# Kernel optimization log

Hardware: AMD Instinct MI355X
Metric: run time of the kernel (lower is better)

Reference implementation:

```python
import jax, jax.numpy as jnp
import numpy as np

BETA = 0.9  # snntorch Leaky beta (single-step, zero init mem => mem = x)
H = 8       # num_heads
EPS = 1e-5

@jax.custom_vjp
def lif_spike(x):
    # snn.Leaky single step, mem init 0: mem = BETA*0 + x ; spk = heaviside(mem - 1.0)
    return (x > 1.0).astype(x.dtype)

def _lif_fwd(x):
    return lif_spike(x), x

def _lif_bwd(x, g):
    # ATan surrogate (snntorch default, alpha=2): d spk/d mem = 1/(1 + (pi*(mem-1))^2)
    u = x - 1.0
    return (g / (1.0 + (jnp.pi * u) ** 2),)

lif_spike.defvjp(_lif_fwd, _lif_bwd)

def layer_norm(x, g, b):
    m = jnp.mean(x, -1, keepdims=True)
    v = jnp.mean((x - m) ** 2, -1, keepdims=True)
    return (x - m) * jax.lax.rsqrt(v + EPS) * g + b

def mha(x, Wqkv, Wo, causal):
    B, N, D = x.shape
    hd = D // H
    q, k, v = jnp.split(x @ Wqkv, 3, axis=-1)
    q = q.reshape(B, N, H, hd).transpose(0, 2, 1, 3)
    k = k.reshape(B, N, H, hd).transpose(0, 2, 1, 3)
    v = v.reshape(B, N, H, hd).transpose(0, 2, 1, 3)
    s = jnp.einsum('bhqd,bhkd->bhqk', q, k) / jnp.sqrt(jnp.asarray(hd, x.dtype))
    if causal:
        s = jnp.where(jnp.tril(jnp.ones((N, N), bool)), s, jnp.asarray(-1e9, x.dtype))
    a = jax.nn.softmax(s, axis=-1)
    o = jnp.einsum('bhqk,bhkd->bhqd', a, v).transpose(0, 2, 1, 3).reshape(B, N, D)
    return o @ Wo

def transformer(x, qkv, out, ln1, ff1, ff2, ln2, causal):
    # pre-norm transformer blocks; Encoder non-causal, Decoder causal
    for i in range(qkv.shape[0]):
        x = x + mha(layer_norm(x, ln1[i, 0], ln1[i, 1]), qkv[i], out[i], causal)
        x = x + jax.nn.gelu(layer_norm(x, ln2[i, 0], ln2[i, 1]) @ ff1[i]) @ ff2[i]
    return x

def setup_inputs():
    key = jax.random.key(0)
    B, R, S, D = 8, 90, 240, 256
    enc_depth, pred_depth = 8, 6
    ks = iter(jax.random.split(key, 64))
    def nrm(shape, std):
        return jax.random.normal(next(ks), shape, jnp.float32) * std
    def enc_params(depth):
        return dict(
            qkv=nrm((depth, D, 3 * D), 0.05),
            out=nrm((depth, D, D), 0.05),
            ln1=jnp.stack([jnp.ones((depth, D)), jnp.zeros((depth, D))], 1),
            ff1=nrm((depth, D, 4 * D), 0.05),
            ff2=nrm((depth, 4 * D, D), 0.05),
            ln2=jnp.stack([jnp.ones((depth, D)), jnp.zeros((depth, D))], 1),
        )
    t, s_, p = enc_params(enc_depth), enc_params(enc_depth), enc_params(pred_depth)
    inp = dict(
        x=jax.random.normal(next(ks), (B, R, S), jnp.float32),
        W_embed=nrm((S, D), 0.1), b_embed=jnp.zeros((D,), jnp.float32),
        pos_embedding=nrm((1, R, D), 1.0),
        mask_token=nrm((1, 1, D), 0.02),
        norm_g=jnp.ones((D,), jnp.float32), norm_b=jnp.zeros((D,), jnp.float32),
        W_dec=nrm((D, S), 0.1), b_dec=jnp.zeros((S,), jnp.float32),
    )
    for name, prm in (('t', t), ('s', s_), ('p', p)):
        for k2, v2 in prm.items():
            inp[name + '_' + k2] = v2
    return inp

def reference(x, W_embed, b_embed, pos_embedding, mask_token, norm_g, norm_b, W_dec, b_dec,
              t_qkv, t_out, t_ln1, t_ff1, t_ff2, t_ln2,
              s_qkv, s_out, s_ln1, s_ff1, s_ff2, s_ln2,
              p_qkv, p_out, p_ln1, p_ff1, p_ff2, p_ln2):
    B, R, S = x.shape
    D = W_embed.shape[1]
    # token embed + pos + token_lif
    x_emb = lif_spike(x @ W_embed + b_embed + pos_embedding)  # [B,R,D]
    # teacher (torch.no_grad)
    teacher_full = lif_spike(layer_norm(
        transformer(x_emb, t_qkv, t_out, t_ln1, t_ff1, t_ff2, t_ln2, False), norm_g, norm_b))
    teacher_full = jax.lax.stop_gradient(teacher_full)
    # student
    student_full = lif_spike(layer_norm(
        transformer(x_emb, s_qkv, s_out, s_ln1, s_ff1, s_ff2, s_ln2, False), norm_g, norm_b))
    # batched exhaustive leave-one-out: for each target t, context = all rows != t
    loo = np.stack([np.delete(np.arange(R), t) for t in range(R)])  # [R, R-1]
    ctx = student_full[:, loo, :]                                   # [B,R,R-1,D]
    masks = lif_spike(mask_token + pos_embedding)                   # [1,R,D] mask_lif
    masks = jnp.broadcast_to(masks[:, :, None, :], (B, R, 1, D))
    seq = jnp.concatenate([ctx, masks], axis=2).reshape(B * R, R, D)
    pred = lif_spike(transformer(seq, p_qkv, p_out, p_ln1, p_ff1, p_ff2, p_ln2, True))
    pred_targets = pred[:, -1, :].reshape(B, R, D)  # last token = predicted target region
    teacher_targets = teacher_full                   # exhaustive: targets are all R rows in order
    pred_seq = lif_spike(pred_targets @ W_dec + b_dec)      # output_lif [B,R,S]
    teacher_seq = lif_spike(teacher_targets @ W_dec + b_dec)
    target_seq = x
    return (pred_seq, teacher_seq, target_seq,
            pred_seq.mean(-1), teacher_seq.mean(-1), target_seq.mean(-1))
```

## Files before the change

kernel.cpp:

```cpp
#include <hip/hip_runtime.h>
#include <math.h>


__device__ __forceinline__ float gelu_f(float x) {
    const float c = 0.7978845608028654f;
    float x3 = x * x * x;
    float inner = c * (x + 0.044715f * x3);
    return 0.5f * x * (1.0f + tanhf(inner));
}

__device__ __forceinline__ int suffix_off(int g) {
    int b = g / 90, r = g - b * 90;
    return b * 4095 + 90 * r - ((r * (r - 1)) >> 1);
}

__global__ __launch_bounds__(256) void embed_kernel(
    const float* __restrict__ x, const float* __restrict__ We,
    const float* __restrict__ be, const float* __restrict__ pos,
    float* __restrict__ xemb) {
    int tok = blockIdx.x;
    int d = threadIdx.x;
    __shared__ float xs[240];
    if (d < 240) xs[d] = x[(size_t)tok * 240 + d];
    __syncthreads();
    int r = tok % 90;
    double acc = 0.0;
    for (int s = 0; s < 240; ++s)
        acc = fma((double)xs[s], (double)We[(size_t)s * 256 + d], acc);
    float a = (float)acc + be[d] + pos[r * 256 + d];
    xemb[(size_t)tok * 256 + d] = (a > 1.0f) ? 1.0f : 0.0f;
}

__global__ void copy_kernel(float* __restrict__ dst, const float* __restrict__ src, int n) {
    int i = blockIdx.x * 256 + threadIdx.x;
    if (i < n) dst[i] = src[i];
}
__global__ void zero_kernel(float* __restrict__ p, int n) {
    int i = blockIdx.x * 256 + threadIdx.x;
    if (i < n) p[i] = 0.f;
}

__global__ __launch_bounds__(256) void ln_kernel(
    const float* __restrict__ X,
    const float* __restrict__ gA, const float* __restrict__ bA,
    const float* __restrict__ gB, const float* __restrict__ bB,
    int split, float* __restrict__ Y) {
    int row = blockIdx.x;
    int d = threadIdx.x;
    const float* g = (row < split) ? gA : gB;
    const float* b = (row < split) ? bA : bB;
    __shared__ float red[256];
    float v = X[(size_t)row * 256 + d];
    red[d] = v;
    __syncthreads();
    for (int s = 128; s > 0; s >>= 1) { if (d < s) red[d] += red[d + s]; __syncthreads(); }
    float mean = red[0] * (1.0f / 256.0f);
    __syncthreads();
    float dv = v - mean;
    red[d] = dv * dv;
    __syncthreads();
    for (int s = 128; s > 0; s >>= 1) { if (d < s) red[d] += red[d + s]; __syncthreads(); }
    float var = red[0] * (1.0f / 256.0f);
    float r = 1.0f / sqrtf(var + 1e-5f);
    Y[(size_t)row * 256 + d] = dv * r * g[d] + b[d];
}

__global__ __launch_bounds__(256) void ln_lif_kernel(
    const float* __restrict__ X, const float* __restrict__ g, const float* __restrict__ b,
    float* __restrict__ Y) {
    int row = blockIdx.x;
    int d = threadIdx.x;
    __shared__ float red[256];
    float v = X[(size_t)row * 256 + d];
    red[d] = v;
    __syncthreads();
    for (int s = 128; s > 0; s >>= 1) { if (d < s) red[d] += red[d + s]; __syncthreads(); }
    float mean = red[0] * (1.0f / 256.0f);
    __syncthreads();
    float dv = v - mean;
    red[d] = dv * dv;
    __syncthreads();
    for (int s = 128; s > 0; s >>= 1) { if (d < s) red[d] += red[d + s]; __syncthreads(); }
    float var = red[0] * (1.0f / 256.0f);
    float r = 1.0f / sqrtf(var + 1e-5f);
    float val = dv * r * g[d] + b[d];
    Y[(size_t)row * 256 + d] = (val > 1.0f) ? 1.0f : 0.0f;
}

#define BM 64
#define BN 64
#define BK 16
template <int EPI>
__global__ __launch_bounds__(256) void gemm_kernel(
    const float* __restrict__ A, const float* __restrict__ W0,
    const float* __restrict__ W1, int wsplit,
    float* __restrict__ C, const float* __restrict__ R,
    int M, int N, int K, int ldA, int ldW, int ldC,
    int zA, int zW, long zC) {
    __shared__ float As[BK][BM + 4];
    __shared__ float Ws[BK][BN];
    int bm = blockIdx.y * BM;
    int bn = blockIdx.x * BN;
    int z = blockIdx.z;
    A += (size_t)z * zA;
    const float* W = ((bm < wsplit) ? W0 : W1) + (size_t)z * zW;
    C += (size_t)z * zC;
    const float* Rp = R + (size_t)z * zC;
    int tid = threadIdx.x;
    int tx = tid & 15;
    int ty = tid >> 4;
    float acc[4][4] = {{0.f}};
    for (int k0 = 0; k0 < K; k0 += BK) {
        {
            int r = tid >> 2;
            int kk = (tid & 3) * 4;
            int gm = bm + r;
            float4 v = make_float4(0.f, 0.f, 0.f, 0.f);
            if (gm < M) v = *(const float4*)(A + (size_t)gm * ldA + k0 + kk);
            As[kk + 0][r] = v.x; As[kk + 1][r] = v.y;
            As[kk + 2][r] = v.z; As[kk + 3][r] = v.w;
        }
        {
            int kk = tid >> 4;
            int n = (tid & 15) * 4;
            float4 v = *(const float4*)(W + (size_t)(k0 + kk) * ldW + bn + n);
            *(float4*)&Ws[kk][n] = v;
        }
        __syncthreads();
        #pragma unroll
        for (int k = 0; k < BK; ++k) {
            float a[4], w[4];
            #pragma unroll
            for (int i = 0; i < 4; ++i) a[i] = As[k][ty * 4 + i];
            #pragma unroll
            for (int j = 0; j < 4; ++j) w[j] = Ws[k][tx * 4 + j];
            #pragma unroll
            for (int i = 0; i < 4; ++i)
                #pragma unroll
                for (int j = 0; j < 4; ++j)
                    acc[i][j] = fmaf(a[i], w[j], acc[i][j]);
        }
        __syncthreads();
    }
    #pragma unroll
    for (int i = 0; i < 4; ++i) {
        int gm = bm + ty * 4 + i;
        if (gm >= M) continue;
        #pragma unroll
        for (int j = 0; j < 4; ++j) {
            int gn = bn + tx * 4 + j;
            float v = acc[i][j];
            if (EPI == 1) v += Rp[(size_t)gm * ldC + gn];
            if (EPI == 2) v = gelu_f(v);
            C[(size_t)gm * ldC + gn] = v;
        }
    }
}

__global__ void addff_kernel(float4* __restrict__ X, const float4* __restrict__ S,
                             long zstr4, int n4) {
    int i = blockIdx.x * 256 + threadIdx.x;
    if (i >= n4) return;
    float4 x = X[i];
    float4 s0 = S[i], s1 = S[i + zstr4], s2 = S[i + 2 * zstr4], s3 = S[i + 3 * zstr4];
    x.x = (((x.x + s0.x) + s1.x) + s2.x) + s3.x;
    x.y = (((x.y + s0.y) + s1.y) + s2.y) + s3.y;
    x.z = (((x.z + s0.z) + s1.z) + s2.z) + s3.z;
    x.w = (((x.w + s0.w) + s1.w) + s2.w) + s3.w;
    X[i] = x;
}

__global__ __launch_bounds__(128) void attn_kernel(
    const float* __restrict__ QKV, float* __restrict__ AO,
    int N, int causal, int hs, int off2) {
    int s = blockIdx.x, h = blockIdx.y;
    int tokbase = (s < hs) ? s * N : off2 + (s - hs) * N;
    __shared__ float Ks[90][32];
    __shared__ float Vs[90][32];
    int tid = threadIdx.x;
    for (int i = tid; i < N * 32; i += 128) {
        int n = i >> 5, d = i & 31;
        size_t base = ((size_t)(tokbase + n)) * 768 + h * 32;
        Ks[n][d] = QKV[base + 256 + d];
        Vs[n][d] = QKV[base + 512 + d];
    }
    __syncthreads();
    int q = tid;
    if (q >= N) return;
    float qv[32];
    size_t qbase = ((size_t)(tokbase + q)) * 768 + h * 32;
    #pragma unroll
    for (int d = 0; d < 32; ++d) qv[d] = QKV[qbase + d];
    const float sq = 5.656854249492380195f;
    int kmax = causal ? (q + 1) : N;
    float m = -3.0e38f;
    for (int k = 0; k < kmax; ++k) {
        float sd = 0.f;
        #pragma unroll
        for (int d = 0; d < 32; ++d) sd = fmaf(qv[d], Ks[k][d], sd);
        sd /= sq;
        m = fmaxf(m, sd);
    }
    float sum = 0.f;
    float acc[32];
    #pragma unroll
    for (int d = 0; d < 32; ++d) acc[d] = 0.f;
    for (int k = 0; k < kmax; ++k) {
        float sd = 0.f;
        #pragma unroll
        for (int d = 0; d < 32; ++d) sd = fmaf(qv[d], Ks[k][d], sd);
        sd /= sq;
        float p = expf(sd - m);
        sum += p;
        #pragma unroll
        for (int d = 0; d < 32; ++d) acc[d] = fmaf(p, Vs[k][d], acc[d]);
    }
    size_t obase = ((size_t)(tokbase + q)) * 256 + h * 32;
    #pragma unroll
    for (int d = 0; d < 32; ++d) AO[obase + d] = acc[d] / sum;
}

__global__ __launch_bounds__(128) void suffix_attn_kernel(
    const float* __restrict__ QKV, const float* __restrict__ kv,
    float* __restrict__ AO, int g0) {
    int ls = blockIdx.x, h = blockIdx.y;
    int g = g0 + ls;
    int b = g / 90, r = g - b * 90;
    int toff = suffix_off(g) - suffix_off(g0);
    int L = 90 - r;
    __shared__ float Ks[90][32];
    __shared__ float Vs[90][32];
    int tid = threadIdx.x;
    for (int i = tid; i < 90 * 32; i += 128) {
        int p = i >> 5, d = i & 31;
        float kk, vv;
        if (p < r) {
            const float* src = kv + ((size_t)(b * 89 + p)) * 512 + h * 32 + d;
            kk = src[0]; vv = src[256];
        } else {
            size_t base = ((size_t)(toff + p - r)) * 768 + h * 32 + d;
            kk = QKV[base + 256]; vv = QKV[base + 512];
        }
        Ks[p][d] = kk; Vs[p][d] = vv;
    }
    __syncthreads();
    if (tid >= L) return;
    int jq = r + tid;
    float qv[32];
    size_t qbase = ((size_t)(toff + tid)) * 768 + h * 32;
    #pragma unroll
    for (int d = 0; d < 32; ++d) qv[d] = QKV[qbase + d];
    const float sq = 5.656854249492380195f;
    int kmax = jq + 1;
    float m = -3.0e38f;
    for (int k = 0; k < kmax; ++k) {
        float sd = 0.f;
        #pragma unroll
        for (int d = 0; d < 32; ++d) sd = fmaf(qv[d], Ks[k][d], sd);
        sd /= sq;
        m = fmaxf(m, sd);
    }
    float sum = 0.f;
    float acc[32];
    #pragma unroll
    for (int d = 0; d < 32; ++d) acc[d] = 0.f;
    for (int k = 0; k < kmax; ++k) {
        float sd = 0.f;
        #pragma unroll
        for (int d = 0; d < 32; ++d) sd = fmaf(qv[d], Ks[k][d], sd);
        sd /= sq;
        float p = expf(sd - m);
        sum += p;
        #pragma unroll
        for (int d = 0; d < 32; ++d) acc[d] = fmaf(p, Vs[k][d], acc[d]);
    }
    size_t obase = ((size_t)(toff + tid)) * 256 + h * 32;
    #pragma unroll
    for (int d = 0; d < 32; ++d) AO[obase + d] = acc[d] / sum;
}

__global__ void masks_kernel(const float* __restrict__ mt, const float* __restrict__ pos,
                             float* __restrict__ M) {
    int i = blockIdx.x * 256 + threadIdx.x;
    if (i >= 90 * 256) return;
    int d = i & 255;
    float v = mt[d] + pos[i];
    M[i] = (v > 1.0f) ? 1.0f : 0.0f;
}

__global__ __launch_bounds__(256) void gather_canon_kernel(
    const float* __restrict__ student, float* __restrict__ Xc, int b0) {
    int tc = blockIdx.x;
    int d = threadIdx.x;
    int b = b0 + tc / 89, p = tc % 89;
    Xc[(size_t)tc * 256 + d] = student[((size_t)(b * 90 + p)) * 256 + d];
}

__global__ __launch_bounds__(256) void kvcopy_kernel(
    const float* __restrict__ QKVc, float* __restrict__ kvl, int b0) {
    int tc = blockIdx.x;
    int c = threadIdx.x;
    size_t gtc = (size_t)b0 * 89 + tc;
    kvl[gtc * 512 + c]       = QKVc[(size_t)tc * 768 + 256 + c];
    kvl[gtc * 512 + 256 + c] = QKVc[(size_t)tc * 768 + 512 + c];
}

__global__ __launch_bounds__(256) void gather_suffix_kernel(
    const float* __restrict__ student, const float* __restrict__ masks,
    float* __restrict__ X, int g0) {
    int ls = blockIdx.x, slot = blockIdx.y;
    int d = threadIdx.x;
    int g = g0 + ls;
    int b = g / 90, r = g - b * 90;
    if (slot >= 90 - r) return;
    int j = r + slot;
    int dst = suffix_off(g) - suffix_off(g0) + slot;
    float v;
    if (j == 89) v = masks[r * 256 + d];
    else         v = student[((size_t)(b * 90 + j + 1)) * 256 + d];
    X[(size_t)dst * 256 + d] = v;
}

__global__ __launch_bounds__(256) void extract_suffix_kernel(
    const float* __restrict__ X, float* __restrict__ predT, int g0) {
    int ls = blockIdx.x;
    int d = threadIdx.x;
    int g = g0 + ls;
    int r = g % 90;
    int tok = suffix_off(g) - suffix_off(g0) + (89 - r);
    float v = X[(size_t)tok * 256 + d];
    predT[(size_t)g * 256 + d] = (v > 1.0f) ? 1.0f : 0.0f;
}

__global__ __launch_bounds__(256) void decode_kernel(
    const float* __restrict__ T, const float* __restrict__ Wd, const float* __restrict__ bd,
    float* __restrict__ outseq, float* __restrict__ outmean) {
    int row = blockIdx.x;
    int n = threadIdx.x;
    __shared__ float ts[256];
    __shared__ float red[256];
    ts[n] = T[(size_t)row * 256 + n];
    __syncthreads();
    float sval = 0.f;
    if (n < 240) {
        double acc = 0.0;
        for (int k = 0; k < 256; ++k)
            acc = fma((double)ts[k], (double)Wd[(size_t)k * 240 + n], acc);
        float a = (float)acc;
        a += bd[n];
        sval = (a > 1.0f) ? 1.0f : 0.0f;
        outseq[(size_t)row * 240 + n] = sval;
    }
    red[n] = sval;
    __syncthreads();
    for (int s = 128; s > 0; s >>= 1) { if (n < s) red[n] += red[n + s]; __syncthreads(); }
    if (n == 0) outmean[row] = red[0] * (1.0f / 240.0f);
}

__global__ __launch_bounds__(256) void target_kernel(
    const float* __restrict__ x, float* __restrict__ outseq, float* __restrict__ outmean) {
    int row = blockIdx.x;
    int n = threadIdx.x;
    __shared__ float red[256];
    float v = 0.f;
    if (n < 240) {
        v = x[(size_t)row * 240 + n];
        outseq[(size_t)row * 240 + n] = v;
    }
    red[n] = v;
    __syncthreads();
    for (int s = 128; s > 0; s >>= 1) { if (n < s) red[n] += red[n + s]; __syncthreads(); }
    if (n == 0) outmean[row] = red[0] * (1.0f / 240.0f);
}

extern "C" void kernel_launch(void* const* d_in, const int* in_sizes, int n_in,
                              void* d_out, int out_size, void* d_ws, size_t ws_size,
                              hipStream_t stream) {
    const float* x   = (const float*)d_in[0];
    const float* We  = (const float*)d_in[1];
    const float* be  = (const float*)d_in[2];
    const float* pos = (const float*)d_in[3];
    const float* mt  = (const float*)d_in[4];
    const float* ng  = (const float*)d_in[5];
    const float* nb  = (const float*)d_in[6];
    const float* Wd  = (const float*)d_in[7];
    const float* bd  = (const float*)d_in[8];
    const float* prm[3][6];
    for (int g = 0; g < 3; ++g)
        for (int k = 0; k < 6; ++k)
            prm[g][k] = (const float*)d_in[9 + g * 6 + k];

    float* wp = (float*)d_ws;
    auto alloc = [&](size_t n) { float* q = wp; wp += n; return q; };
    float* x_emb   = alloc(720 * 256);
    float* teacher = alloc(720 * 256);
    float* student = alloc(720 * 256);
    float* predT   = alloc(720 * 256);
    float* masksb  = alloc(90 * 256);
    float* kvc     = alloc(6ull * 712 * 512);
    size_t fixed = (size_t)(wp - (float*)d_ws);

    size_t avail = ws_size / 4;
    long tcap_l = 90;
    if (avail > fixed) {
        long t = (long)((avail - fixed) / 3328);
        if (t > tcap_l) tcap_l = t;
    }
    if (tcap_l > 32760) tcap_l = 32760;
    int TCAP = (int)tcap_l;
    float* X   = alloc((size_t)TCAP * 256);
    float* Xn  = alloc((size_t)TCAP * 256);
    float* QKV = alloc((size_t)TCAP * 768);
    float* H   = alloc((size_t)TCAP * 1024);
    float* S   = alloc(4ull * TCAP * 256);
    long  zS   = (long)TCAP * 256;
    bool co_batch = (TCAP >= 1488);

    float* out = (float*)d_out;
    const int NOSPLIT = 1 << 30;

    embed_kernel<<<720, 256, 0, stream>>>(x, We, be, pos, x_emb);
    masks_kernel<<<90, 256, 0, stream>>>(mt, pos, masksb);

    auto run_layer = [&](int T, int gA, int gB, int l, int split, auto&& attn_launch) {
        const float* qkvA = prm[gA][0] + (size_t)l * 256 * 768;
        const float* qkvB = prm[gB][0] + (size_t)l * 256 * 768;
        const float* woA  = prm[gA][1] + (size_t)l * 256 * 256;
        const float* woB  = prm[gB][1] + (size_t)l * 256 * 256;
        const float* l1A  = prm[gA][2] + (size_t)l * 512;
        const float* l1B  = prm[gB][2] + (size_t)l * 512;
        const float* f1A  = prm[gA][3] + (size_t)l * 256 * 1024;
        const float* f1B  = prm[gB][3] + (size_t)l * 256 * 1024;
        const float* f2A  = prm[gA][4] + (size_t)l * 1024 * 256;
        const float* f2B  = prm[gB][4] + (size_t)l * 1024 * 256;
        const float* l2A  = prm[gA][5] + (size_t)l * 512;
        const float* l2B  = prm[gB][5] + (size_t)l * 512;
        int gy = (T + 63) / 64;
        ln_kernel<<<T, 256, 0, stream>>>(X, l1A, l1A + 256, l1B, l1B + 256, split, Xn);
        gemm_kernel<0><<<dim3(12, gy, 1), 256, 0, stream>>>(
            Xn, qkvA, qkvB, split, QKV, QKV, T, 768, 256, 256, 768, 768, 0, 0, 0);
        attn_launch();
        gemm_kernel<1><<<dim3(4, gy, 1), 256, 0, stream>>>(
            Xn, woA, woB, split, X, X, T, 256, 256, 256, 256, 256, 0, 0, 0);
        ln_kernel<<<T, 256, 0, stream>>>(X, l2A, l2A + 256, l2B, l2B + 256, split, Xn);
        gemm_kernel<2><<<dim3(16, gy, 1), 256, 0, stream>>>(
            Xn, f1A, f1B, split, H, H, T, 1024, 256, 256, 1024, 1024, 0, 0, 0);
        gemm_kernel<0><<<dim3(4, gy, 4), 256, 0, stream>>>(
            H, f2A, f2B, split, S, S, T, 256, 256, 1024, 256, 256, 256, 65536, zS);
        addff_kernel<<<(T * 64 + 255) / 256, 256, 0, stream>>>(
            (float4*)X, (const float4*)S, zS / 4, T * 64);
    };

    if (co_batch) {
        copy_kernel<<<720, 256, 0, stream>>>(X, x_emb, 720 * 256);
        copy_kernel<<<720, 256, 0, stream>>>(X + 768 * 256, x_emb, 720 * 256);
        zero_kernel<<<48, 256, 0, stream>>>(X + 720 * 256, 48 * 256);
        for (int l = 0; l < 8; ++l)
            run_layer(1488, 0, 1, l, 768,
                      [&] { attn_kernel<<<dim3(16, 8), 128, 0, stream>>>(
                                QKV, Xn, 90, 0, 8, 768); });
        ln_lif_kernel<<<720, 256, 0, stream>>>(X, ng, nb, teacher);
        ln_lif_kernel<<<720, 256, 0, stream>>>(X + 768 * 256, ng, nb, student);
    } else {
        int ce = TCAP / 90; if (ce > 8) ce = 8; if (ce < 1) ce = 1;
        for (int gi = 0; gi < 2; ++gi) {
            for (int s0 = 0; s0 < 8; s0 += ce) {
                int c = (8 - s0) < ce ? (8 - s0) : ce;
                int T = c * 90;
                copy_kernel<<<(T * 256 + 255) / 256, 256, 0, stream>>>(
                    X, x_emb + (size_t)s0 * 90 * 256, T * 256);
                for (int l = 0; l < 8; ++l)
                    run_layer(T, gi, gi, l, NOSPLIT,
                              [&] { attn_kernel<<<dim3(c, 8), 128, 0, stream>>>(
                                        QKV, Xn, 90, 0, c, 0); });
                ln_lif_kernel<<<T, 256, 0, stream>>>(
                    X, ng, nb, (gi == 0 ? teacher : student) + (size_t)s0 * 90 * 256);
            }
        }
    }

    {
        int cb = TCAP / 89; if (cb > 8) cb = 8; if (cb < 1) cb = 1;
        for (int b0 = 0; b0 < 8; b0 += cb) {
            int c = (8 - b0) < cb ? (8 - b0) : cb;
            int T = c * 89;
            gather_canon_kernel<<<T, 256, 0, stream>>>(student, X, b0);
            for (int l = 0; l < 6; ++l) {
                float* kvl = kvc + (size_t)l * 712 * 512;
                run_layer(T, 2, 2, l, NOSPLIT,
                          [&] {
                              kvcopy_kernel<<<T, 256, 0, stream>>>(QKV, kvl, b0);
                              attn_kernel<<<dim3(c, 8), 128, 0, stream>>>(
                                  QKV, Xn, 89, 1, c, 0);
                          });
            }
        }
    }

    auto Toff = [](int g) { int b = g / 90, r = g - b * 90;
                            return (long)b * 4095 + 90L * r - (long)r * (r - 1) / 2; };
    int cs = TCAP / 90; if (cs < 1) cs = 1; if (cs > 720) cs = 720;
    for (int g0 = 0; g0 < 720; ) {
        int g1 = g0 + cs; if (g1 > 720) g1 = 720;
        while ((int)(Toff(g1) - Toff(g0)) > TCAP && g1 > g0 + 1) --g1;
        int c = g1 - g0;
        int Tc = (int)(Toff(g1) - Toff(g0));
        { dim3 g(c, 90);
          gather_suffix_kernel<<<g, 256, 0, stream>>>(student, masksb, X, g0); }
        for (int l = 0; l < 6; ++l) {
            float* kvl = kvc + (size_t)l * 712 * 512;
            run_layer(Tc, 2, 2, l, NOSPLIT,
                      [&] { dim3 g(c, 8);
                            suffix_attn_kernel<<<g, 128, 0, stream>>>(QKV, kvl, Xn, g0); });
        }
        extract_suffix_kernel<<<c, 256, 0, stream>>>(X, predT, g0);
        g0 = g1;
    }

    decode_kernel<<<720, 256, 0, stream>>>(predT, Wd, bd, out + 0, out + 518400);
    decode_kernel<<<720, 256, 0, stream>>>(teacher, Wd, bd, out + 172800, out + 519120);
    target_kernel<<<720, 256, 0, stream>>>(x, out + 345600, out + 519840);
}
```

Measured before the change: 9.874 ms.

## Compute only last-token rows in final predictor layer; double-buffer GEMM smem

The last predictor layer only matters at the final (mask) token, so the suffix path now runs QKV for all tokens but attention, output projection, LN2 and FFN only for the last row of each sequence, using a new single-query attention kernel. The canonical-prefix pass in the last layer now only computes K/V without the full layer. The GEMM kernel also gets register-prefetch double-buffering of shared-memory tiles to overlap global loads with FMA work. This adds workspace buffers and more launches per chunk, and the last-query attention uses a single thread per head, which may be slow.

```diff
diff --git a/kernel.cpp b/kernel.cpp
--- a/kernel.cpp
+++ b/kernel.cpp
@@ -87,8 +87,6 @@
     Y[(size_t)row * 256 + d] = (val > 1.0f) ? 1.0f : 0.0f;
 }
 
-#define BM 64
-#define BN 64
 #define BK 16
 template <int EPI>
 __global__ __launch_bounds__(256) void gemm_kernel(
@@ -97,10 +95,10 @@
     float* __restrict__ C, const float* __restrict__ R,
     int M, int N, int K, int ldA, int ldW, int ldC,
     int zA, int zW, long zC) {
-    __shared__ float As[BK][BM + 4];
-    __shared__ float Ws[BK][BN];
-    int bm = blockIdx.y * BM;
-    int bn = blockIdx.x * BN;
+    __shared__ float As[2][BK][64 + 4];
+    __shared__ float Ws[2][BK][64];
+    int bm = blockIdx.y * 64;
+    int bn = blockIdx.x * 64;
     int z = blockIdx.z;
     A += (size_t)z * zA;
     const float* W = ((bm < wsplit) ? W0 : W1) + (size_t)z * zW;
@@ -109,50 +107,63 @@
     int tid = threadIdx.x;
     int tx = tid & 15;
     int ty = tid >> 4;
+    int ar = tid >> 2;
+    int ak = (tid & 3) * 4;
+    int wk = tid >> 4;
+    int wn = (tid & 15) * 4;
+    int gm = bm + ar;
+    bool aok = gm < M;
+    const float* Aptr = A + (size_t)gm * ldA + ak;
+    const float* Wptr = W + (size_t)wk * ldW + bn + wn;
+
     float acc[4][4] = {{0.f}};
-    for (int k0 = 0; k0 < K; k0 += BK) {
-        {
-            int r = tid >> 2;
-            int kk = (tid & 3) * 4;
-            int gm = bm + r;
-            float4 v = make_float4(0.f, 0.f, 0.f, 0.f);
-            if (gm < M) v = *(const float4*)(A + (size_t)gm * ldA + k0 + kk);
-            As[kk + 0][r] = v.x; As[kk + 1][r] = v.y;
-            As[kk + 2][r] = v.z; As[kk + 3][r] = v.w;
-        }
-        {
-            int kk = tid >> 4;
-            int n = (tid & 15) * 4;
-            float4 v = *(const float4*)(W + (size_t)(k0 + kk) * ldW + bn + n);
-            *(float4*)&Ws[kk][n] = v;
-        }
-        __syncthreads();
+    float4 va = aok ? *(const float4*)Aptr : make_float4(0.f, 0.f, 0.f, 0.f);
+    float4 vw = *(const float4*)Wptr;
+    As[0][ak + 0][ar] = va.x; As[0][ak + 1][ar] = va.y;
+    As[0][ak + 2][ar] = va.z; As[0][ak + 3][ar] = va.w;
+    *(float4*)&Ws[0][wk][wn] = vw;
+    __syncthreads();
+
+    int nt = K / BK;
+    for (int t = 0; t < nt; ++t) {
+        int cur = t & 1;
+        if (t + 1 < nt) {
+            va = aok ? *(const float4*)(Aptr + (t + 1) * BK)
+                     : make_float4(0.f, 0.f, 0.f, 0.f);
+            vw = *(const float4*)(Wptr + (size_t)(t + 1) * BK * ldW);
+        }
         #pragma unroll
         for (int k = 0; k < BK; ++k) {
             float a[4], w[4];
             #pragma unroll
-            for (int i = 0; i < 4; ++i) a[i] = As[k][ty * 4 + i];
+            for (int i = 0; i < 4; ++i) a[i] = As[cur][k][ty * 4 + i];
             #pragma unroll
-            for (int j = 0; j < 4; ++j) w[j] = Ws[k][tx * 4 + j];
+            for (int j = 0; j < 4; ++j) w[j] = Ws[cur][k][tx * 4 + j];
             #pragma unroll
             for (int i = 0; i < 4; ++i)
                 #pragma unroll
                 for (int j = 0; j < 4; ++j)
                     acc[i][j] = fmaf(a[i], w[j], acc[i][j]);
         }
+        if (t + 1 < nt) {
+            int nx = cur ^ 1;
+            As[nx][ak + 0][ar] = va.x; As[nx][ak + 1][ar] = va.y;
+            As[nx][ak + 2][ar] = va.z; As[nx][ak + 3][ar] = va.w;
+            *(float4*)&Ws[nx][wk][wn] = vw;
+        }
         __syncthreads();
     }
     #pragma unroll
     for (int i = 0; i < 4; ++i) {
-        int gm = bm + ty * 4 + i;
-        if (gm >= M) continue;
+        int om = bm + ty * 4 + i;
+        if (om >= M) continue;
         #pragma unroll
         for (int j = 0; j < 4; ++j) {
-            int gn = bn + tx * 4 + j;
+            int on = bn + tx * 4 + j;
             float v = acc[i][j];
-            if (EPI == 1) v += Rp[(size_t)gm * ldC + gn];
+            if (EPI == 1) v += Rp[(size_t)om * ldC + on];
             if (EPI == 2) v = gelu_f(v);
-            C[(size_t)gm * ldC + gn] = v;
+            C[(size_t)om * ldC + on] = v;
         }
     }
 }
@@ -279,6 +290,63 @@
     for (int d = 0; d < 32; ++d) AO[obase + d] = acc[d] / sum;
 }
 
+__global__ __launch_bounds__(128) void lastq_attn_kernel(
+    const float* __restrict__ QKV, const float* __restrict__ kv,
+    float* __restrict__ AO2, int g0) {
+    int ls = blockIdx.x, h = blockIdx.y;
+    int g = g0 + ls;
+    int b = g / 90, r = g - b * 90;
+    int toff = suffix_off(g) - suffix_off(g0);
+    int L = 90 - r;
+    __shared__ float Ks[90][32];
+    __shared__ float Vs[90][32];
+    int tid = threadIdx.x;
+    for (int i = tid; i < 90 * 32; i += 128) {
+        int p = i >> 5, d = i & 31;
+        float kk, vv;
+        if (p < r) {
+            const float* src = kv + ((size_t)(b * 89 + p)) * 512 + h * 32 + d;
+            kk = src[0]; vv = src[256];
+        } else {
+            size_t base = ((size_t)(toff + p - r)) * 768 + h * 32 + d;
+            kk = QKV[base + 256]; vv = QKV[base + 512];
+        }
+        Ks[p][d] = kk; Vs[p][d] = vv;
+    }
+    __syncthreads();
+    if (tid != 0) return;
+    float qv[32];
+    size_t qbase = ((size_t)(toff + L - 1)) * 768 + h * 32;
+    #pragma unroll
+    for (int d = 0; d < 32; ++d) qv[d] = QKV[qbase + d];
+    const float sq = 5.656854249492380195f;
+    float m = -3.0e38f;
+    for (int k = 0; k < 90; ++k) {
+        float sd = 0.f;
+        #pragma unroll
+        for (int d = 0; d < 32; ++d) sd = fmaf(qv[d], Ks[k][d], sd);
+        sd /= sq;
+        m = fmaxf(m, sd);
+    }
+    float sum = 0.f;
+    float acc[32];
+    #pragma unroll
+    for (int d = 0; d < 32; ++d) acc[d] = 0.f;
+    for (int k = 0; k < 90; ++k) {
+        float sd = 0.f;
+        #pragma unroll
+        for (int d = 0; d < 32; ++d) sd = fmaf(qv[d], Ks[k][d], sd);
+        sd /= sq;
+        float p = expf(sd - m);
+        sum += p;
+        #pragma unroll
+        for (int d = 0; d < 32; ++d) acc[d] = fmaf(p, Vs[k][d], acc[d]);
+    }
+    size_t obase = (size_t)ls * 256 + h * 32;
+    #pragma unroll
+    for (int d = 0; d < 32; ++d) AO2[obase + d] = acc[d] / sum;
+}
+
 __global__ void masks_kernel(const float* __restrict__ mt, const float* __restrict__ pos,
                              float* __restrict__ M) {
     int i = blockIdx.x * 256 + threadIdx.x;
@@ -321,15 +389,22 @@
     X[(size_t)dst * 256 + d] = v;
 }
 
-__global__ __launch_bounds__(256) void extract_suffix_kernel(
-    const float* __restrict__ X, float* __restrict__ predT, int g0) {
+__global__ __launch_bounds__(256) void gather_last_kernel(
+    const float* __restrict__ X, float* __restrict__ X2, int g0) {
     int ls = blockIdx.x;
     int d = threadIdx.x;
     int g = g0 + ls;
     int r = g % 90;
     int tok = suffix_off(g) - suffix_off(g0) + (89 - r);
-    float v = X[(size_t)tok * 256 + d];
-    predT[(size_t)g * 256 + d] = (v > 1.0f) ? 1.0f : 0.0f;
+    X2[(size_t)ls * 256 + d] = X[(size_t)tok * 256 + d];
+}
+
+__global__ __launch_bounds__(256) void lif_rows_kernel(
+    const float* __restrict__ X2, float* __restrict__ predT, int g0) {
+    int ls = blockIdx.x;
+    int d = threadIdx.x;
+    float v = X2[(size_t)ls * 256 + d];
+    predT[(size_t)(g0 + ls) * 256 + d] = (v > 1.0f) ? 1.0f : 0.0f;
 }
 
 __global__ __launch_bounds__(256) void decode_kernel(
@@ -398,6 +473,12 @@
     float* predT   = alloc(720 * 256);
     float* masksb  = alloc(90 * 256);
     float* kvc     = alloc(6ull * 712 * 512);
+    float* AO2 = alloc(720 * 256);
+    float* X2  = alloc(720 * 256);
+    float* Xn2 = alloc(720 * 256);
+    float* H2  = alloc(720 * 1024);
+    float* S2  = alloc(4ull * 720 * 256);
+    long  zS2  = 720 * 256;
     size_t fixed = (size_t)(wp - (float*)d_ws);
 
     size_t avail = ws_size / 4;
@@ -485,7 +566,7 @@
             int c = (8 - b0) < cb ? (8 - b0) : cb;
             int T = c * 89;
             gather_canon_kernel<<<T, 256, 0, stream>>>(student, X, b0);
-            for (int l = 0; l < 6; ++l) {
+            for (int l = 0; l < 5; ++l) {
                 float* kvl = kvc + (size_t)l * 712 * 512;
                 run_layer(T, 2, 2, l, NOSPLIT,
                           [&] {
@@ -493,6 +574,17 @@
                               attn_kernel<<<dim3(c, 8), 128, 0, stream>>>(
                                   QKV, Xn, 89, 1, c, 0);
                           });
+            }
+            {
+                const float* l1P  = prm[2][2] + 5ull * 512;
+                const float* qkvP = prm[2][0] + 5ull * 256 * 768;
+                float* kvl = kvc + 5ull * 712 * 512;
+                int gy = (T + 63) / 64;
+                ln_kernel<<<T, 256, 0, stream>>>(X, l1P, l1P + 256, l1P, l1P + 256,
+                                                 NOSPLIT, Xn);
+                gemm_kernel<0><<<dim3(12, gy, 1), 256, 0, stream>>>(
+                    Xn, qkvP, qkvP, NOSPLIT, QKV, QKV, T, 768, 256, 256, 768, 768, 0, 0, 0);
+                kvcopy_kernel<<<T, 256, 0, stream>>>(QKV, kvl, b0);
             }
         }
     }
@@ -507,13 +599,41 @@
         int Tc = (int)(Toff(g1) - Toff(g0));
         { dim3 g(c, 90);
           gather_suffix_kernel<<<g, 256, 0, stream>>>(student, masksb, X, g0); }
-        for (int l = 0; l < 6; ++l) {
+        for (int l = 0; l < 5; ++l) {
             float* kvl = kvc + (size_t)l * 712 * 512;
             run_layer(Tc, 2, 2, l, NOSPLIT,
                       [&] { dim3 g(c, 8);
                             suffix_attn_kernel<<<g, 128, 0, stream>>>(QKV, kvl, Xn, g0); });
         }
-        extract_suffix_kernel<<<c, 256, 0, stream>>>(X, predT, g0);
+        {
+            const float* qkvP = prm[2][0] + 5ull * 256 * 768;
+            const float* woP  = prm[2][1] + 5ull * 256 * 256;
+            const float* l1P  = prm[2][2] + 5ull * 512;
+            const float* f1P  = prm[2][3] + 5ull * 256 * 1024;
+            const float* f2P  = prm[2][4] + 5ull * 1024 * 256;
+            const float* l2P  = prm[2][5] + 5ull * 512;
+            float* kvl = kvc + 5ull * 712 * 512;
+            int gy  = (Tc + 63) / 64;
+            int gyc = (c + 63) / 64;
+            ln_kernel<<<Tc, 256, 0, stream>>>(X, l1P, l1P + 256, l1P, l1P + 256,
+                                              NOSPLIT, Xn);
+            gemm_kernel<0><<<dim3(12, gy, 1), 256, 0, stream>>>(
+                Xn, qkvP, qkvP, NOSPLIT, QKV, QKV, Tc, 768, 256, 256, 768, 768, 0, 0, 0);
+            { dim3 g(c, 8);
+              lastq_attn_kernel<<<g, 128, 0, stream>>>(QKV, kvl, AO2, g0); }
+            gather_last_kernel<<<c, 256, 0, stream>>>(X, X2, g0);
+            gemm_kernel<1><<<dim3(4, gyc, 1), 256, 0, stream>>>(
+                AO2, woP, woP, NOSPLIT, X2, X2, c, 256, 256, 256, 256, 256, 0, 0, 0);
+            ln_kernel<<<c, 256, 0, stream>>>(X2, l2P, l2P + 256, l2P, l2P + 256,
+                                             NOSPLIT, Xn2);
+            gemm_kernel<2><<<dim3(16, gyc, 1), 256, 0, stream>>>(
+                Xn2, f1P, f1P, NOSPLIT, H2, H2, c, 1024, 256, 256, 1024, 1024, 0, 0, 0);
+            gemm_kernel<0><<<dim3(4, gyc, 4), 256, 0, stream>>>(
+                H2, f2P, f2P, NOSPLIT, S2, S2, c, 256, 256, 1024, 256, 256, 256, 65536, zS2);
+            addff_kernel<<<(c * 64 + 255) / 256, 256, 0, stream>>>(
+                (float4*)X2, (const float4*)S2, zS2 / 4, c * 64);
+            lif_rows_kernel<<<c, 256, 0, stream>>>(X2, predT, g0);
+        }
         g0 = g1;
     }
 
```

Result: faster. 9.435 ms (-4.4%).
